# Kernel optimization log

Hardware: AMD Instinct MI355X
Metric: run time of the kernel (lower is better)

Reference implementation:

```python
import jax, jax.numpy as jnp
import numpy as np

N = 30000
F_IN = 500
HID = 16
OUT = 3
E = 960000


def setup_inputs() -> dict:
    key = jax.random.key(0)
    ks = jax.random.split(key, 10)
    x = jax.random.normal(ks[0], (N, F_IN), dtype=jnp.float32)
    edge_index = jax.random.randint(ks[1], (2, E), 0, N, dtype=jnp.int32)
    # CNN params (torch Conv1d: weight [out, in, k], bias [out])
    s1 = 1.0 / np.sqrt(1 * 3)
    s2 = 1.0 / np.sqrt(HID * 3)
    conv1_w = jax.random.uniform(ks[2], (HID, 1, 3), jnp.float32, -s1, s1)
    conv1_b = jax.random.uniform(ks[3], (HID,), jnp.float32, -s1, s1)
    conv2_w = jax.random.uniform(ks[4], (HID, HID, 3), jnp.float32, -s2, s2)
    conv2_b = jax.random.uniform(ks[5], (HID,), jnp.float32, -s2, s2)
    # GCNConv params (glorot weight [in, out], zero bias)
    g1 = np.sqrt(6.0 / (HID + HID))
    g2 = np.sqrt(6.0 / (HID + OUT))
    gcn1_w = jax.random.uniform(ks[6], (HID, HID), jnp.float32, -g1, g1)
    gcn1_b = jnp.zeros((HID,), jnp.float32)
    gcn2_w = jax.random.uniform(ks[7], (HID, OUT), jnp.float32, -g2, g2)
    gcn2_b = jnp.zeros((OUT,), jnp.float32)
    return {"x": x, "conv1_w": conv1_w, "conv1_b": conv1_b,
            "conv2_w": conv2_w, "conv2_b": conv2_b,
            "gcn1_w": gcn1_w, "gcn1_b": gcn1_b,
            "gcn2_w": gcn2_w, "gcn2_b": gcn2_b,
            "edge_index": edge_index}


def _conv1d(x, w, b):
    # x: [N, C_in, L], w: [C_out, C_in, 3], padding=1
    y = jax.lax.conv_general_dilated(
        x, w, window_strides=(1,), padding=[(1, 1)],
        dimension_numbers=("NCH", "OIH", "NCH"))
    return y + b[None, :, None]


def _gcn_conv(x, w, b, src, dst, n):
    # x: [n, d_in] -> [n, d_out]; Kipf normalization with self-loops
    h = x @ w
    loop = jnp.arange(n, dtype=src.dtype)
    s = jnp.concatenate([src, loop])
    d = jnp.concatenate([dst, loop])
    deg = jax.ops.segment_sum(jnp.ones_like(d, dtype=h.dtype), d, num_segments=n)
    dinv = jnp.where(deg > 0, jax.lax.rsqrt(deg), 0.0)
    norm = dinv[s] * dinv[d]                      # [E+n]
    msg = h[s] * norm[:, None]                    # gather + scale
    return jax.ops.segment_sum(msg, d, num_segments=n) + b


def reference(x, conv1_w, conv1_b, conv2_w, conv2_b,
              gcn1_w, gcn1_b, gcn2_w, gcn2_b, edge_index):
    # CNN feature extractor over feature axis
    h = x[:, None, :]                             # [N, 1, F_IN]
    h = jax.nn.relu(_conv1d(h, conv1_w, conv1_b))  # [N, HID, F_IN]
    h = jax.nn.relu(_conv1d(h, conv2_w, conv2_b))  # [N, HID, F_IN]
    h = jnp.max(h, axis=2)                        # global max pool -> [N, HID]
    # GCN
    src, dst = edge_index[0], edge_index[1]
    n = h.shape[0]
    h = jax.nn.relu(_gcn_conv(h, gcn1_w, gcn1_b, src, dst, n))
    h = _gcn_conv(h, gcn2_w, gcn2_b, src, dst, n)  # [N, OUT]
    return jax.nn.log_softmax(h, axis=1)
```

## Files before the change

### kernel.cpp

```cpp
#include <hip/hip_runtime.h>
#include <hip/hip_bf16.h>

#define N_NODES 30000
#define F_INLEN 500
#define HID 16
#define OUTC 3
#define NEDGE 960000
#define YPITCH 20
#define NBIN 938
#define HBLK 128
#define EPRH (NEDGE / HBLK)
#define ECAP 1536
#define NPB2 235

typedef float  f32x4 __attribute__((ext_vector_type(4)));
typedef float  f32x2 __attribute__((ext_vector_type(2)));
typedef short  s16x8 __attribute__((ext_vector_type(8)));

static __device__ __forceinline__ unsigned short f2bf(float f) {
    unsigned int u = __float_as_uint(f);
    unsigned int r = (u + 0x7fffu + ((u >> 16) & 1u)) >> 16;
    return (unsigned short)r;
}
static __device__ __forceinline__ unsigned int pack_bf16x2(float v0, float v1) {
#if __has_builtin(__builtin_amdgcn_cvt_pk_bf16_f32)
    typedef __bf16 bf16x2_t __attribute__((ext_vector_type(2)));
    union { bf16x2_t v; unsigned int u; } cv;
    cv.v = __builtin_amdgcn_cvt_pk_bf16_f32(v0, v1);
    return cv.u;
#else
    return __builtin_amdgcn_perm(__float_as_uint(v1), __float_as_uint(v0), 0x07060302);
#endif
}

__global__ void setup_kernel(const float* __restrict__ w2, short* __restrict__ bfragsG)
{
    const int tid = threadIdx.x;
    const int n16 = tid & 15, q = tid >> 4;
#pragma unroll
    for (int j = 0; j < 8; j++) {
        {
            const int c = q * 8 + j;
            const int t = c >> 4, i = c & 15;
            bfragsG[tid * 16 + j] = (short)f2bf(w2[n16 * 48 + i * 3 + t]);
        }
        {
            const int c = 32 + q * 8 + j;
            short v = 0;
            if (c < 48) { const int t = c >> 4, i = c & 15; v = (short)f2bf(w2[n16 * 48 + i * 3 + t]); }
            bfragsG[tid * 16 + 8 + j] = v;
        }
    }
}

__global__ __launch_bounds__(256, 7) void conv_hist(
    const float* __restrict__ x,
    const float* __restrict__ w1, const float* __restrict__ b1,
    const float* __restrict__ b2, const short* __restrict__ bfragsG,
    const int* __restrict__ dst, int* __restrict__ degi,
    int* __restrict__ cntbase, float* __restrict__ h0)
{
    __shared__ __align__(16) float xp[502];
    __shared__ __align__(16) unsigned short yh[516 * YPITCH];
    __shared__ float red[64];

    const int tid = threadIdx.x;

    if (blockIdx.x < HBLK) {
        int* histH = (int*)yh;
        for (int i = tid; i < NBIN; i += 256) histH[i] = 0;
        __syncthreads();
        const int e0 = blockIdx.x * EPRH;
        for (int e = e0 + tid; e < e0 + EPRH; e += 256) {
            const int d = dst[e];
            atomicAdd(&histH[d >> 5], 1);
            atomicAdd(&degi[d], 1);
        }
        __syncthreads();
        for (int i = tid; i < NBIN; i += 256) cntbase[blockIdx.x * NBIN + i] = histH[i];
        return;
    }

    const int node = blockIdx.x - HBLK;
    const int lane = tid & 63;
    const int wave = tid >> 6;
    const int n16  = lane & 15;
    const int q    = lane >> 4;

    if (tid == 0) { xp[0] = 0.f; xp[501] = 0.f; }
    if (tid < 125) {
        const float4 v = ((const float4*)(x + (long long)node * F_INLEN))[tid];
        xp[4 * tid + 1] = v.x; xp[4 * tid + 2] = v.y;
        xp[4 * tid + 3] = v.z; xp[4 * tid + 4] = v.w;
    }
    {
        const int ri = tid >> 4;
        const int row = (ri == 0) ? 0 : (500 + ri);
        yh[row * YPITCH + (tid & 15)] = 0;
    }
    const s16x8* bfp = (const s16x8*)(bfragsG + lane * 16);
    const s16x8 bh0 = bfp[0], bh1 = bfp[1];

    f32x2 wt0[8], wt1[8], wt2[8], bb[8];
#pragma unroll
    for (int cp = 0; cp < 8; cp++) {
        const int c0 = 2 * cp, c1 = 2 * cp + 1;
        wt0[cp] = (f32x2){w1[c0 * 3 + 0], w1[c1 * 3 + 0]};
        wt1[cp] = (f32x2){w1[c0 * 3 + 1], w1[c1 * 3 + 1]};
        wt2[cp] = (f32x2){w1[c0 * 3 + 2], w1[c1 * 3 + 2]};
        bb[cp]  = (f32x2){b1[c0], b1[c1]};
    }
    __syncthreads();

    for (int p = tid; p < 500; p += 256) {
        const float x0 = xp[p], x1 = xp[p + 1], x2 = xp[p + 2];
        const f32x2 xv0 = {x0, x0}, xv1 = {x1, x1}, xv2 = {x2, x2};
        const f32x2 zero = {0.f, 0.f};
        unsigned int hp[8];
#pragma unroll
        for (int cp = 0; cp < 8; cp++) {
            f32x2 a = bb[cp];
            a = __builtin_elementwise_fma(wt0[cp], xv0, a);
            a = __builtin_elementwise_fma(wt1[cp], xv1, a);
            a = __builtin_elementwise_fma(wt2[cp], xv2, a);
            a = __builtin_elementwise_max(a, zero);
            hp[cp] = pack_bf16x2(a[0], a[1]);
        }
        uint2* d = (uint2*)&yh[(p + 1) * YPITCH];
        d[0] = make_uint2(hp[0], hp[1]);
        d[1] = make_uint2(hp[2], hp[3]);
        d[2] = make_uint2(hp[4], hp[5]);
        d[3] = make_uint2(hp[6], hp[7]);
    }
    __syncthreads();

    struct S8 { short4 lo, hi; };
    float mx0 = -3.0e38f, mx1 = -3.0e38f, mx2 = -3.0e38f, mx3 = -3.0e38f;
#pragma unroll
    for (int it = 0; it < 8; it++) {
        const int tile = wave * 8 + it;
        const int p0 = tile * 16 + n16;
        const int cA = (q & 1) * 8;
        const int rA = p0 + (q >> 1);
        const int rB = p0 + 2 + (q >> 1);
        S8 t0, t1;
        t0.lo = *(const short4*)&yh[rA * YPITCH + cA];
        t0.hi = *(const short4*)&yh[rA * YPITCH + cA + 4];
        t1.lo = *(const short4*)&yh[rB * YPITCH + cA];
        t1.hi = *(const short4*)&yh[rB * YPITCH + cA + 4];
        const s16x8 ah0 = *(const s16x8*)&t0;
        const s16x8 ah1 = *(const s16x8*)&t1;
        f32x4 acc = {0.f, 0.f, 0.f, 0.f};
        acc = __builtin_amdgcn_mfma_f32_16x16x32_bf16(ah0, bh0, acc, 0, 0, 0);
        acc = __builtin_amdgcn_mfma_f32_16x16x32_bf16(ah1, bh1, acc, 0, 0, 0);
        if (it < 7) {
            mx0 = fmaxf(mx0, acc[0]);
            mx1 = fmaxf(mx1, acc[1]);
            mx2 = fmaxf(mx2, acc[2]);
            mx3 = fmaxf(mx3, acc[3]);
        } else if (wave < 3) {
            mx0 = fmaxf(mx0, acc[0]);
            mx1 = fmaxf(mx1, acc[1]);
            mx2 = fmaxf(mx2, acc[2]);
            mx3 = fmaxf(mx3, acc[3]);
        } else if (q == 0) {
            mx0 = fmaxf(mx0, acc[0]);
            mx1 = fmaxf(mx1, acc[1]);
            mx2 = fmaxf(mx2, acc[2]);
            mx3 = fmaxf(mx3, acc[3]);
        }
    }
    float m = fmaxf(fmaxf(mx0, mx1), fmaxf(mx2, mx3));
    m = fmaxf(m, __shfl_xor(m, 16));
    m = fmaxf(m, __shfl_xor(m, 32));
    if (lane < 16) red[wave * 16 + lane] = m;
    __syncthreads();
    if (tid < 16) {
        const float mm = fmaxf(fmaxf(red[tid], red[16 + tid]), fmaxf(red[32 + tid], red[48 + tid]));
        h0[node * HID + tid] = fmaxf(mm + b2[tid], 0.f);
    }
}

__global__ __launch_bounds__(512) void reorder2(
    const int* __restrict__ src, const int* __restrict__ dst,
    const int* __restrict__ cntbase, int* __restrict__ packed,
    int* __restrict__ binstart, const int* __restrict__ degi,
    float* __restrict__ dinv, float* __restrict__ h0)
{
    __shared__ int2 sc2A[NBIN], sc2B[NBIN];
    __shared__ int gexc[NBIN];
    __shared__ int lexc[NBIN];
    __shared__ int cursor[NBIN];
    __shared__ int srt[EPRH];
    const int tid = threadIdx.x;
    const int blk = blockIdx.x;

    for (int bin = tid; bin < NBIN; bin += 512) {
        int tot = 0, psum = 0, lc = 0;
        for (int k = 0; k < HBLK; k++) {
            const int c = cntbase[k * NBIN + bin];
            tot += c;
            if (k < blk) psum += c;
            if (k == blk) lc = c;
        }
        cursor[bin] = tot;
        gexc[bin]   = psum;
        lexc[bin]   = lc;
        sc2A[bin]   = make_int2(tot, lc);
    }
    __syncthreads();
    {
        int2* pA = sc2A; int2* pB = sc2B;
        for (int off = 1; off < NBIN; off <<= 1) {
            for (int i = tid; i < NBIN; i += 512) {
                int2 v = pA[i];
                if (i >= off) { const int2 u = pA[i - off]; v.x += u.x; v.y += u.y; }
                pB[i] = v;
            }
            __syncthreads();
            int2* tp = pA; pA = pB; pB = tp;
        }
        for (int i = tid; i < NBIN; i += 512) {
            const int tot = cursor[i];
            const int lc  = lexc[i];
            const int et  = pA[i].x - tot;
            const int el  = pA[i].y - lc;
            gexc[i] += et;
            if (blk == 0) binstart[i] = et;
            lexc[i]   = el;
            cursor[i] = el;
        }
        if (blk == 0 && tid == 0) binstart[NBIN] = NEDGE;
    }
    __syncthreads();
    const int e0 = blk * EPRH;
    for (int e = e0 + tid; e < e0 + EPRH; e += 512) {
        const int d = dst[e];
        const int bin = d >> 5;
        const int pos = atomicAdd(&cursor[bin], 1);
        srt[pos] = src[e] | (d << 15);
    }
    __syncthreads();
    for (int i = tid; i < EPRH; i += 512) {
        const int bin = srt[i] >> 20;
        packed[gexc[bin] + (i - lexc[bin])] = srt[i];
    }
    const int n0 = blk * NPB2;
    for (int n = n0 + tid; n < n0 + NPB2 && n < N_NODES; n += 512) {
        const float dv = rsqrtf((float)(degi[n] + 1));
        dinv[n] = dv;
        f32x4* h4 = (f32x4*)(h0 + n * HID);
#pragma unroll
        for (int k = 0; k < 4; k++) h4[k] = h4[k] * dv;
    }
}

__global__ __launch_bounds__(256) void agg1_kernel(
    const int* __restrict__ binstart, int* __restrict__ packed,
    const float* __restrict__ h0,
    const float* __restrict__ W1, const float* __restrict__ b1g,
    const float* __restrict__ W2, float4* __restrict__ t2p4,
    int* __restrict__ binofs)
{
    __shared__ float w1s[256];
    __shared__ float w2s[48];
    __shared__ float b1s[16];
    __shared__ float accS[32 * 17];
    __shared__ int eL[ECAP];
    __shared__ int srt[ECAP];
    __shared__ int h32[32], ls32[32], lofs32[32];
    const int tid = threadIdx.x;
    const int blk = blockIdx.x;
    w1s[tid] = W1[tid];
    if (tid < 48) w2s[tid] = W2[tid];
    if (tid < 16) b1s[tid] = b1g[tid];
    if (tid < 32) h32[tid] = 0;
    const int beg = binstart[blk];
    const int cnt = binstart[blk + 1] - beg;
    __syncthreads();
    for (int j = tid; j < cnt; j += 256) {
        const int p = packed[beg + j];
        eL[j] = p;
        atomicAdd(&h32[(p >> 15) & 31], 1);
    }
    __syncthreads();
    if (tid < 32) {
        const int v = h32[tid];
        int inc = v;
#pragma unroll
        for (int off = 1; off < 32; off <<= 1) {
            const int y = __shfl_up(inc, off);
            if (tid >= off) inc += y;
        }
        ls32[tid] = inc - v;
        lofs32[tid] = inc - v;
    }
    __syncthreads();
    for (int j = tid; j < cnt; j += 256) {
        const int p = eL[j];
        const int pos = atomicAdd(&lofs32[(p >> 15) & 31], 1);
        srt[pos] = p;
    }
    __syncthreads();
    for (int j = tid; j < cnt; j += 256) packed[beg + j] = srt[j];
    if (tid < 32) {
        binofs[blk * 64 + tid]      = ls32[tid];
        binofs[blk * 64 + 32 + tid] = h32[tid];
    }
    const int n = tid >> 3;
    const int eslot = (tid >> 2) & 1;
    const int q = tid & 3;
    const int node = blk * 32 + n;
    const bool valid = node < N_NODES;
    f32x4 acc = {0.f, 0.f, 0.f, 0.f};
    if (valid) {
        const int s0 = ls32[n];
        const int s1 = s0 + h32[n];
        for (int i = s0 + eslot; i < s1; i += 2) {
            const int s = srt[i] & 32767;
            acc += *(const f32x4*)(h0 + s * HID + q * 4);
        }
    }
#pragma unroll
    for (int c = 0; c < 4; c++) acc[c] += __shfl_xor(acc[c], 4);
    if (valid && eslot == 0) {
        acc += *(const f32x4*)(h0 + node * HID + q * 4);
        accS[n * 17 + q * 4 + 0] = acc[0];
        accS[n * 17 + q * 4 + 1] = acc[1];
        accS[n * 17 + q * 4 + 2] = acc[2];
        accS[n * 17 + q * 4 + 3] = acc[3];
    }
    __syncthreads();
    if (tid < 128) {
        const int n2 = tid >> 2;
        const int node2 = blk * 32 + n2;
        if (node2 < N_NODES) {
            const float dv = rsqrtf((float)(h32[n2] + 1));
            const int q2 = tid & 3;
            float y0 = 0.f, y1 = 0.f, y2 = 0.f, y3 = 0.f;
#pragma unroll
            for (int i = 0; i < 16; i++) {
                const float a = accS[n2 * 17 + i];
                y0 = fmaf(a, w1s[i * 16 + q2 * 4 + 0], y0);
                y1 = fmaf(a, w1s[i * 16 + q2 * 4 + 1], y1);
                y2 = fmaf(a, w1s[i * 16 + q2 * 4 + 2], y2);
                y3 = fmaf(a, w1s[i * 16 + q2 * 4 + 3], y3);
            }
            float d0 = 0.f, d1 = 0.f, d2 = 0.f;
            const float yv[4] = {y0, y1, y2, y3};
#pragma unroll
            for (int j = 0; j < 4; j++) {
                const int o = q2 * 4 + j;
                const float h = fmaxf(b1s[o] + dv * yv[j], 0.f);
                d0 = fmaf(h, w2s[o * 3 + 0], d0);
                d1 = fmaf(h, w2s[o * 3 + 1], d1);
                d2 = fmaf(h, w2s[o * 3 + 2], d2);
            }
            d0 += __shfl_xor(d0, 1); d0 += __shfl_xor(d0, 2);
            d1 += __shfl_xor(d1, 1); d1 += __shfl_xor(d1, 2);
            d2 += __shfl_xor(d2, 1); d2 += __shfl_xor(d2, 2);
            if (q2 == 0) t2p4[node2] = make_float4(d0 * dv, d1 * dv, d2 * dv, dv);
        }
    }
}

__global__ __launch_bounds__(256) void agg2_kernel(
    const int* __restrict__ binstart, const int* __restrict__ packed,
    const float4* __restrict__ t2p4, const int* __restrict__ binofs,
    const float* __restrict__ b2g, float* __restrict__ out)
{
    __shared__ int eL[ECAP];
    __shared__ int ofs[64];
    const int tid = threadIdx.x;
    const int blk = blockIdx.x;
    const int beg = binstart[blk];
    const int cnt = binstart[blk + 1] - beg;
    if (tid < 64) ofs[tid] = binofs[blk * 64 + tid];
    for (int j = tid; j < cnt; j += 256) eL[j] = packed[beg + j];
    __syncthreads();
    const int n = tid >> 3;
    const int ln8 = tid & 7;
    const int node = blk * 32 + n;
    float a0 = 0.f, a1 = 0.f, a2 = 0.f;
    if (node < N_NODES) {
        const int s0 = ofs[n];
        const int s1 = s0 + ofs[32 + n];
        for (int i = s0 + ln8; i < s1; i += 8) {
            const int s = eL[i] & 32767;
            const float4 v = t2p4[s];
            a0 += v.x; a1 += v.y; a2 += v.z;
        }
    }
#pragma unroll
    for (int msk = 1; msk < 8; msk <<= 1) {
        a0 += __shfl_xor(a0, msk);
        a1 += __shfl_xor(a1, msk);
        a2 += __shfl_xor(a2, msk);
    }
    if (ln8 == 0 && node < N_NODES) {
        const float4 self = t2p4[node];
        const float dv = self.w;
        const float z0 = b2g[0] + dv * (a0 + self.x);
        const float z1 = b2g[1] + dv * (a1 + self.y);
        const float z2 = b2g[2] + dv * (a2 + self.z);
        const float m = fmaxf(z0, fmaxf(z1, z2));
        const float lg = m + logf(expf(z0 - m) + expf(z1 - m) + expf(z2 - m));
        out[node * 3 + 0] = z0 - lg;
        out[node * 3 + 1] = z1 - lg;
        out[node * 3 + 2] = z2 - lg;
    }
}

extern "C" void kernel_launch(void* const* d_in, const int* in_sizes, int n_in,
                              void* d_out, int out_size, void* d_ws, size_t ws_size,
                              hipStream_t stream)
{
    const float* x   = (const float*)d_in[0];
    const float* w1  = (const float*)d_in[1];
    const float* b1  = (const float*)d_in[2];
    const float* w2  = (const float*)d_in[3];
    const float* b2  = (const float*)d_in[4];
    const float* g1w = (const float*)d_in[5];
    const float* g1b = (const float*)d_in[6];
    const float* g2w = (const float*)d_in[7];
    const float* g2b = (const float*)d_in[8];
    const int*   ei  = (const int*)d_in[9];
    const int* src = ei;
    const int* dst = ei + NEDGE;

    float* ws = (float*)d_ws;
    float*  h0      = ws;
    float*  dinv    = ws + 480000;
    float4* t2p4    = (float4*)(ws + 510000);
    int*    degi    = (int*)(ws + 630000);
    int*    cntbase = (int*)(ws + 660000);
    int*    binstart= (int*)(ws + 780064);
    int*    packed  = (int*)(ws + 781024);
    int*    binofs  = (int*)(ws + 1741024);
    short*  bfragsG = (short*)(ws + 1801056);
    float*  out     = (float*)d_out;

    hipMemsetAsync(degi, 0, N_NODES * sizeof(int), stream);
    setup_kernel<<<1, 64, 0, stream>>>(w2, bfragsG);
    conv_hist<<<HBLK + N_NODES, 256, 0, stream>>>(x, w1, b1, b2, bfragsG,
                                                  dst, degi, cntbase, h0);
    reorder2<<<HBLK, 512, 0, stream>>>(src, dst, cntbase, packed, binstart,
                                       degi, dinv, h0);
    agg1_kernel<<<NBIN, 256, 0, stream>>>(binstart, packed, h0,
                                          g1w, g1b, g2w, t2p4, binofs);
    agg2_kernel<<<NBIN, 256, 0, stream>>>(binstart, packed, t2p4, binofs, g2b, out);
}
```

Baseline: 229.5 us.

## Move histogram ahead of conv and overlap edge reordering with conv blocks

The histogram pass moves into its own kernel, merged with the weight-fragment setup, so it runs before the conv. The conv kernel's extra blocks then do the prefix scan and scatter edges straight into packed global order, in parallel with the conv blocks. The separate reorder kernel is gone, and the degree normalization is folded into the conv epilogue, so there is one fewer launch and no extra pass over h0. The cost is that the scatter now writes directly to global memory with atomics and no shared-memory staging, so writes are less coalesced, and the histogram now runs serially before the conv instead of overlapping it.

```diff
diff --git a/kernel.cpp b/kernel.cpp
--- a/kernel.cpp
+++ b/kernel.cpp
@@ -11,7 +11,6 @@
 #define HBLK 128
 #define EPRH (NEDGE / HBLK)
 #define ECAP 1536
-#define NPB2 235
 
 typedef float  f32x4 __attribute__((ext_vector_type(4)));
 typedef float  f32x2 __attribute__((ext_vector_type(2)));
@@ -33,32 +32,52 @@
 #endif
 }
 
-__global__ void setup_kernel(const float* __restrict__ w2, short* __restrict__ bfragsG)
+__global__ __launch_bounds__(256) void hist_kernel(
+    const float* __restrict__ w2, short* __restrict__ bfragsG,
+    const int* __restrict__ dst, int* __restrict__ degi, int* __restrict__ cntbase)
 {
     const int tid = threadIdx.x;
-    const int n16 = tid & 15, q = tid >> 4;
-#pragma unroll
-    for (int j = 0; j < 8; j++) {
-        {
-            const int c = q * 8 + j;
-            const int t = c >> 4, i = c & 15;
-            bfragsG[tid * 16 + j] = (short)f2bf(w2[n16 * 48 + i * 3 + t]);
-        }
-        {
-            const int c = 32 + q * 8 + j;
-            short v = 0;
-            if (c < 48) { const int t = c >> 4, i = c & 15; v = (short)f2bf(w2[n16 * 48 + i * 3 + t]); }
-            bfragsG[tid * 16 + 8 + j] = v;
-        }
-    }
-}
-
-__global__ __launch_bounds__(256, 7) void conv_hist(
+    if (blockIdx.x == HBLK) {
+        if (tid < 64) {
+            const int n16 = tid & 15, q = tid >> 4;
+#pragma unroll
+            for (int j = 0; j < 8; j++) {
+                {
+                    const int c = q * 8 + j;
+                    const int t = c >> 4, i = c & 15;
+                    bfragsG[tid * 16 + j] = (short)f2bf(w2[n16 * 48 + i * 3 + t]);
+                }
+                {
+                    const int c = 32 + q * 8 + j;
+                    short v = 0;
+                    if (c < 48) { const int t = c >> 4, i = c & 15; v = (short)f2bf(w2[n16 * 48 + i * 3 + t]); }
+                    bfragsG[tid * 16 + 8 + j] = v;
+                }
+            }
+        }
+        return;
+    }
+    __shared__ int histH[NBIN];
+    for (int i = tid; i < NBIN; i += 256) histH[i] = 0;
+    __syncthreads();
+    const int e0 = blockIdx.x * EPRH;
+    for (int e = e0 + tid; e < e0 + EPRH; e += 256) {
+        const int d = dst[e];
+        atomicAdd(&histH[d >> 5], 1);
+        atomicAdd(&degi[d], 1);
+    }
+    __syncthreads();
+    for (int i = tid; i < NBIN; i += 256) cntbase[blockIdx.x * NBIN + i] = histH[i];
+}
+
+__global__ __launch_bounds__(256, 7) void conv_reorder(
     const float* __restrict__ x,
     const float* __restrict__ w1, const float* __restrict__ b1,
     const float* __restrict__ b2, const short* __restrict__ bfragsG,
-    const int* __restrict__ dst, int* __restrict__ degi,
-    int* __restrict__ cntbase, float* __restrict__ h0)
+    const int* __restrict__ src, const int* __restrict__ dst,
+    const int* __restrict__ degi, const int* __restrict__ cntbase,
+    int* __restrict__ packed, int* __restrict__ binstart,
+    float* __restrict__ h0)
 {
     __shared__ __align__(16) float xp[502];
     __shared__ __align__(16) unsigned short yh[516 * YPITCH];
@@ -67,17 +86,43 @@
     const int tid = threadIdx.x;
 
     if (blockIdx.x < HBLK) {
-        int* histH = (int*)yh;
-        for (int i = tid; i < NBIN; i += 256) histH[i] = 0;
+        int* scA    = (int*)yh;
+        int* scB    = scA + NBIN;
+        int* totb   = scB + NBIN;
+        int* cursor = totb + NBIN;
+        const int blk = blockIdx.x;
+        for (int bin = tid; bin < NBIN; bin += 256) {
+            int tot = 0, psum = 0;
+            for (int k = 0; k < HBLK; k++) {
+                const int c = cntbase[k * NBIN + bin];
+                tot += c;
+                if (k < blk) psum += c;
+            }
+            scA[bin]    = tot;
+            totb[bin]   = tot;
+            cursor[bin] = psum;
+        }
         __syncthreads();
-        const int e0 = blockIdx.x * EPRH;
+        int* pA = scA; int* pB = scB;
+        for (int off = 1; off < NBIN; off <<= 1) {
+            for (int i = tid; i < NBIN; i += 256)
+                pB[i] = pA[i] + ((i >= off) ? pA[i - off] : 0);
+            __syncthreads();
+            int* tp = pA; pA = pB; pB = tp;
+        }
+        for (int i = tid; i < NBIN; i += 256) {
+            const int excl = pA[i] - totb[i];
+            cursor[i] += excl;
+            if (blk == 0) binstart[i] = excl;
+        }
+        if (blk == 0 && tid == 0) binstart[NBIN] = NEDGE;
+        __syncthreads();
+        const int e0 = blk * EPRH;
         for (int e = e0 + tid; e < e0 + EPRH; e += 256) {
             const int d = dst[e];
-            atomicAdd(&histH[d >> 5], 1);
-            atomicAdd(&degi[d], 1);
-        }
-        __syncthreads();
-        for (int i = tid; i < NBIN; i += 256) cntbase[blockIdx.x * NBIN + i] = histH[i];
+            const int pos = atomicAdd(&cursor[d >> 5], 1);
+            packed[pos] = src[e] | (d << 15);
+        }
         return;
     }
 
@@ -177,81 +222,8 @@
     __syncthreads();
     if (tid < 16) {
         const float mm = fmaxf(fmaxf(red[tid], red[16 + tid]), fmaxf(red[32 + tid], red[48 + tid]));
-        h0[node * HID + tid] = fmaxf(mm + b2[tid], 0.f);
-    }
-}
-
-__global__ __launch_bounds__(512) void reorder2(
-    const int* __restrict__ src, const int* __restrict__ dst,
-    const int* __restrict__ cntbase, int* __restrict__ packed,
-    int* __restrict__ binstart, const int* __restrict__ degi,
-    float* __restrict__ dinv, float* __restrict__ h0)
-{
-    __shared__ int2 sc2A[NBIN], sc2B[NBIN];
-    __shared__ int gexc[NBIN];
-    __shared__ int lexc[NBIN];
-    __shared__ int cursor[NBIN];
-    __shared__ int srt[EPRH];
-    const int tid = threadIdx.x;
-    const int blk = blockIdx.x;
-
-    for (int bin = tid; bin < NBIN; bin += 512) {
-        int tot = 0, psum = 0, lc = 0;
-        for (int k = 0; k < HBLK; k++) {
-            const int c = cntbase[k * NBIN + bin];
-            tot += c;
-            if (k < blk) psum += c;
-            if (k == blk) lc = c;
-        }
-        cursor[bin] = tot;
-        gexc[bin]   = psum;
-        lexc[bin]   = lc;
-        sc2A[bin]   = make_int2(tot, lc);
-    }
-    __syncthreads();
-    {
-        int2* pA = sc2A; int2* pB = sc2B;
-        for (int off = 1; off < NBIN; off <<= 1) {
-            for (int i = tid; i < NBIN; i += 512) {
-                int2 v = pA[i];
-                if (i >= off) { const int2 u = pA[i - off]; v.x += u.x; v.y += u.y; }
-                pB[i] = v;
-            }
-            __syncthreads();
-            int2* tp = pA; pA = pB; pB = tp;
-        }
-        for (int i = tid; i < NBIN; i += 512) {
-            const int tot = cursor[i];
-            const int lc  = lexc[i];
-            const int et  = pA[i].x - tot;
-            const int el  = pA[i].y - lc;
-            gexc[i] += et;
-            if (blk == 0) binstart[i] = et;
-            lexc[i]   = el;
-            cursor[i] = el;
-        }
-        if (blk == 0 && tid == 0) binstart[NBIN] = NEDGE;
-    }
-    __syncthreads();
-    const int e0 = blk * EPRH;
-    for (int e = e0 + tid; e < e0 + EPRH; e += 512) {
-        const int d = dst[e];
-        const int bin = d >> 5;
-        const int pos = atomicAdd(&cursor[bin], 1);
-        srt[pos] = src[e] | (d << 15);
-    }
-    __syncthreads();
-    for (int i = tid; i < EPRH; i += 512) {
-        const int bin = srt[i] >> 20;
-        packed[gexc[bin] + (i - lexc[bin])] = srt[i];
-    }
-    const int n0 = blk * NPB2;
-    for (int n = n0 + tid; n < n0 + NPB2 && n < N_NODES; n += 512) {
-        const float dv = rsqrtf((float)(degi[n] + 1));
-        dinv[n] = dv;
-        f32x4* h4 = (f32x4*)(h0 + n * HID);
-#pragma unroll
-        for (int k = 0; k < 4; k++) h4[k] = h4[k] * dv;
+        const float dv = rsqrtf((float)(degi[node] + 1));
+        h0[node * HID + tid] = fmaxf(mm + b2[tid], 0.f) * dv;
     }
 }
 
@@ -430,22 +402,20 @@
 
     float* ws = (float*)d_ws;
     float*  h0      = ws;
-    float*  dinv    = ws + 480000;
-    float4* t2p4    = (float4*)(ws + 510000);
-    int*    degi    = (int*)(ws + 630000);
-    int*    cntbase = (int*)(ws + 660000);
-    int*    binstart= (int*)(ws + 780064);
-    int*    packed  = (int*)(ws + 781024);
-    int*    binofs  = (int*)(ws + 1741024);
-    short*  bfragsG = (short*)(ws + 1801056);
+    float4* t2p4    = (float4*)(ws + 480000);
+    int*    degi    = (int*)(ws + 600000);
+    int*    cntbase = (int*)(ws + 630000);
+    int*    binstart= (int*)(ws + 750064);
+    int*    packed  = (int*)(ws + 751104);
+    int*    binofs  = (int*)(ws + 1711104);
+    short*  bfragsG = (short*)(ws + 1771136);
     float*  out     = (float*)d_out;
 
     hipMemsetAsync(degi, 0, N_NODES * sizeof(int), stream);
-    setup_kernel<<<1, 64, 0, stream>>>(w2, bfragsG);
-    conv_hist<<<HBLK + N_NODES, 256, 0, stream>>>(x, w1, b1, b2, bfragsG,
-                                                  dst, degi, cntbase, h0);
-    reorder2<<<HBLK, 512, 0, stream>>>(src, dst, cntbase, packed, binstart,
-                                       degi, dinv, h0);
+    hist_kernel<<<HBLK + 1, 256, 0, stream>>>(w2, bfragsG, dst, degi, cntbase);
+    conv_reorder<<<HBLK + N_NODES, 256, 0, stream>>>(x, w1, b1, b2, bfragsG,
+                                                     src, dst, degi, cntbase,
+                                                     packed, binstart, h0);
     agg1_kernel<<<NBIN, 256, 0, stream>>>(binstart, packed, h0,
                                           g1w, g1b, g2w, t2p4, binofs);
     agg2_kernel<<<NBIN, 256, 0, stream>>>(binstart, packed, t2p4, binofs, g2b, out);
```

New measurement: 223.4 us. 1.03x faster.
